# Optimization experiments

Measured on AMD Instinct MI355X. Metric: run time of the kernel, lower is better.

Reference implementation:

```python
import jax, jax.numpy as jnp
import numpy as np

B, N, D = 8, 1024, 1024
H, DH = 16, 64
INNER = H * DH  # == D by construction
MLP = 4096
EPS = 1e-5


def layernorm(x, g, b):
    mu = jnp.mean(x, axis=-1, keepdims=True)
    var = jnp.mean(jnp.square(x - mu), axis=-1, keepdims=True)
    return (x - mu) * jax.lax.rsqrt(var + EPS) * g + b


def setup_inputs() -> dict:
    key = jax.random.key(0)
    ks = jax.random.split(key, 10)
    s = lambda fan_in: 1.0 / np.sqrt(fan_in)
    return {
        "x": jax.random.normal(ks[0], (B, N, D), jnp.float32),
        "ln1_g": jnp.ones((D,), jnp.float32),
        "ln1_b": jnp.zeros((D,), jnp.float32),
        "w_qkv": jax.random.uniform(ks[1], (D, 3 * INNER), jnp.float32, -s(D), s(D)),
        "w_out": jax.random.uniform(ks[2], (INNER, D), jnp.float32, -s(INNER), s(INNER)),
        "b_out": jnp.zeros((D,), jnp.float32),
        "ln2_g": jnp.ones((D,), jnp.float32),
        "ln2_b": jnp.zeros((D,), jnp.float32),
        "w1": jax.random.uniform(ks[3], (D, MLP), jnp.float32, -s(D), s(D)),
        "b1": jnp.zeros((MLP,), jnp.float32),
        "w2": jax.random.uniform(ks[4], (MLP, D), jnp.float32, -s(MLP), s(MLP)),
        "b2": jnp.zeros((D,), jnp.float32),
    }


def reference(x, ln1_g, ln1_b, w_qkv, w_out, b_out, ln2_g, ln2_b, w1, b1, w2, b2):
    scale = DH ** -0.5
    xn = layernorm(x, ln1_g, ln1_b)
    qkv = xn @ w_qkv  # [B, N, 3*INNER]
    embed_dim = xn.shape[-1]
    # faithful to source: slice by embed_dim (== INNER here)
    q, k, v = (qkv[:, :, embed_dim * i: embed_dim * (i + 1)] for i in range(3))
    reshape_heads = lambda t: t.reshape(B, N, H, DH).transpose(0, 2, 1, 3)  # b h n d
    q, k, v = reshape_heads(q), reshape_heads(k), reshape_heads(v)
    scores = jnp.einsum("bhnd,bhmd->bhnm", q, k) * scale
    attn = jax.nn.softmax(scores, axis=-1)
    attn_out = jnp.einsum("bhnm,bhmd->bhnd", attn, v)
    attn_out = attn_out.transpose(0, 2, 1, 3).reshape(B, N, INNER)
    x2 = attn_out @ w_out + b_out  # to_ff projection (project_out=True)
    # feed_forward: LayerNorm -> Linear -> GELU(exact) -> Linear (dropout=0)
    h = layernorm(x2, ln2_g, ln2_b) @ w1 + b1
    h = jax.nn.gelu(h, approximate=False)
    out = h @ w2 + b2
    return out
```

## Files before the change

### kernel.cpp

```cpp
#include <hip/hip_runtime.h>
#include <hip/hip_bf16.h>
#include <math.h>

typedef __bf16 bf16;
typedef __bf16 bf16x8 __attribute__((ext_vector_type(8)));
typedef float f32x4 __attribute__((ext_vector_type(4)));

#define SEQ 1024
#define DMODEL 1024

__device__ __forceinline__ void gld_lds16(const bf16* g, bf16* l) {
    __builtin_amdgcn_global_load_lds(
        (const __attribute__((address_space(1))) unsigned int*)g,
        (__attribute__((address_space(3))) unsigned int*)l, 16, 0, 0);
}

__global__ void transpose_f2b(const float* __restrict__ in, bf16* __restrict__ out,
                              int K, int N) {
    __shared__ float tile[32][33];
    int n0 = blockIdx.x * 32, k0 = blockIdx.y * 32;
    int tx = threadIdx.x, ty = threadIdx.y;
#pragma unroll
    for (int i = 0; i < 4; ++i) {
        int kk = ty + i * 8;
        tile[kk][tx] = in[(size_t)(k0 + kk) * N + n0 + tx];
    }
    __syncthreads();
#pragma unroll
    for (int i = 0; i < 4; ++i) {
        int nn = ty + i * 8;
        out[(size_t)(n0 + nn) * K + k0 + tx] = (bf16)tile[tx][nn];
    }
}

__global__ void ln_f2b(const float* __restrict__ x, const float* __restrict__ g,
                       const float* __restrict__ bta, bf16* __restrict__ y) {
    int row = blockIdx.x, t = threadIdx.x;
    const float* xr = x + (size_t)row * DMODEL;
    float v[4];
#pragma unroll
    for (int i = 0; i < 4; ++i) v[i] = xr[t * 4 + i];
    float s = v[0] + v[1] + v[2] + v[3];
    float s2 = v[0] * v[0] + v[1] * v[1] + v[2] * v[2] + v[3] * v[3];
#pragma unroll
    for (int off = 32; off > 0; off >>= 1) {
        s += __shfl_down(s, off, 64);
        s2 += __shfl_down(s2, off, 64);
    }
    __shared__ float ws1[4], ws2[4];
    __shared__ float mu_s, rstd_s;
    int lane = t & 63, wv = t >> 6;
    if (lane == 0) { ws1[wv] = s; ws2[wv] = s2; }
    __syncthreads();
    if (t == 0) {
        float S1 = ws1[0] + ws1[1] + ws1[2] + ws1[3];
        float S2 = ws2[0] + ws2[1] + ws2[2] + ws2[3];
        float mu = S1 * (1.0f / DMODEL);
        float var = S2 * (1.0f / DMODEL) - mu * mu;
        mu_s = mu;
        rstd_s = rsqrtf(var + 1e-5f);
    }
    __syncthreads();
    float mu = mu_s, rstd = rstd_s;
    bf16* yr = y + (size_t)row * DMODEL;
#pragma unroll
    for (int i = 0; i < 4; ++i) {
        int d = t * 4 + i;
        float o = (v[i] - mu) * rstd * g[d] + bta[d];
        yr[d] = (bf16)o;
    }
}

#define BM 128
#define BN 128
#define BK 32

__global__ __launch_bounds__(256, 2) void gemm_bt(
    const bf16* __restrict__ A, const bf16* __restrict__ Bt,
    const float* __restrict__ bias, void* __restrict__ Cv,
    int M, int N, int K, int mode) {
    __shared__ bf16 sA[BM * BK];
    __shared__ bf16 sB[BN * BK];
    int t = threadIdx.x;
    int lane = t & 63, wave = t >> 6;
    int wr = wave >> 1, wc = wave & 1;
    int m0 = blockIdx.y * BM, n0 = blockIdx.x * BN;
    const bf16* Ap = A + (size_t)m0 * K;
    const bf16* Bp = Bt + (size_t)n0 * K;

    int srow = wave * 16 + (lane >> 2);
    int schunk = lane & 3;
    int gcoff = (schunk ^ (srow & 3)) * 8;
    const bf16* gA0 = Ap + (size_t)srow * K + gcoff;
    const bf16* gA1 = Ap + (size_t)(srow + 64) * K + gcoff;
    const bf16* gB0 = Bp + (size_t)srow * K + gcoff;
    const bf16* gB1 = Bp + (size_t)(srow + 64) * K + gcoff;
    bf16* lA0 = sA + wave * 512;
    bf16* lA1 = sA + 2048 + wave * 512;
    bf16* lB0 = sB + wave * 512;
    bf16* lB1 = sB + 2048 + wave * 512;

    f32x4 acc[4][4];
#pragma unroll
    for (int i = 0; i < 4; ++i)
#pragma unroll
        for (int j = 0; j < 4; ++j) acc[i][j] = (f32x4){0.f, 0.f, 0.f, 0.f};

    int mq = lane & 15, quad = lane >> 4;
    int csw = (quad ^ (mq & 3)) * 8;

    for (int k0 = 0; k0 < K; k0 += BK) {
        __syncthreads();
        gld_lds16(gA0 + k0, lA0);
        gld_lds16(gA1 + k0, lA1);
        gld_lds16(gB0 + k0, lB0);
        gld_lds16(gB1 + k0, lB1);
        __syncthreads();
        bf16x8 af[4], bfr[4];
#pragma unroll
        for (int i = 0; i < 4; ++i)
            af[i] = *(const bf16x8*)&sA[(wr * 64 + i * 16 + mq) * BK + csw];
#pragma unroll
        for (int j = 0; j < 4; ++j)
            bfr[j] = *(const bf16x8*)&sB[(wc * 64 + j * 16 + mq) * BK + csw];
#pragma unroll
        for (int i = 0; i < 4; ++i)
#pragma unroll
            for (int j = 0; j < 4; ++j)
                acc[i][j] = __builtin_amdgcn_mfma_f32_16x16x32_bf16(af[i], bfr[j], acc[i][j], 0, 0, 0);
    }

    int cq = lane & 15, rq = (lane >> 4) * 4;
#pragma unroll
    for (int i = 0; i < 4; ++i) {
        int row = m0 + wr * 64 + i * 16 + rq;
#pragma unroll
        for (int j = 0; j < 4; ++j) {
            int col = n0 + wc * 64 + j * 16 + cq;
            float bv = bias ? bias[col] : 0.0f;
#pragma unroll
            for (int r = 0; r < 4; ++r) {
                float v = acc[i][j][r] + bv;
                if (mode == 1) v = 0.5f * v * (1.0f + erff(v * 0.70710678118654752f));
                size_t idx = (size_t)(row + r) * N + col;
                if (mode == 2) ((float*)Cv)[idx] = v;
                else           ((bf16*)Cv)[idx] = (bf16)v;
            }
        }
    }
}

#define GBAR() do { asm volatile("" ::: "memory"); __builtin_amdgcn_sched_barrier(0); \
    __builtin_amdgcn_s_barrier(); __builtin_amdgcn_sched_barrier(0); asm volatile("" ::: "memory"); } while (0)
#define GWAITV2() do { asm volatile("s_waitcnt vmcnt(2)" ::: "memory"); __builtin_amdgcn_sched_barrier(0); } while (0)
#define GWAITV0() do { asm volatile("s_waitcnt vmcnt(0)" ::: "memory"); __builtin_amdgcn_sched_barrier(0); } while (0)

__global__ __launch_bounds__(512, 2) void gemm256_bt(
    const bf16* __restrict__ A, const bf16* __restrict__ Bt,
    const float* __restrict__ bias, void* __restrict__ Cv,
    int M, int N, int K, int mode) {
    extern __shared__ bf16 smem[];
    int t = threadIdx.x;
    int lane = t & 63, wave = t >> 6;
    int wr = wave >> 2, wc = wave & 3;

    int nbx = gridDim.x;
    int nwg = nbx * (int)gridDim.y;
    int bid = (int)blockIdx.y * nbx + (int)blockIdx.x;
    int qd = nwg >> 3, rm = nwg & 7;
    int xcd = bid & 7, loc = bid >> 3;
    int wg = (xcd < rm ? xcd * (qd + 1) : rm * (qd + 1) + (xcd - rm) * qd) + loc;
    int m0 = (wg / nbx) * 256, n0 = (wg % nbx) * 256;

    const bf16* Ap = A + (size_t)m0 * K;
    const bf16* Bp = Bt + (size_t)n0 * K;

    int sr = lane >> 3;
    int g8 = lane & 7;
    int soff = (g8 ^ (sr & 7)) * 8;
    const bf16* gA = Ap + (size_t)(wave * 8 + sr) * K + soff;
    const bf16* gB = Bp + (size_t)(wave * 8 + sr) * K + soff;

    int mq = lane & 15, quad = lane >> 4;
    int fro = (quad ^ (mq & 7)) * 8;

    f32x4 acc[8][4];
#pragma unroll
    for (int i = 0; i < 8; ++i)
#pragma unroll
        for (int j = 0; j < 4; ++j) acc[i][j] = (f32x4){0.f, 0.f, 0.f, 0.f};

    bf16x8 af[4][2], bq[2][2];
    const bf16 *sA, *sB;
    int nt = K >> 6;

#define SMP(b, ab) (smem + ((size_t)((b) * 2 + (ab))) * 16384)
#define STG(b, cl, tt) do { \
    gld_lds16(gA + (size_t)(cl) * 64 * K + (size_t)(tt) * 64, SMP(b, 0) + ((cl) * 64 + wave * 8) * 64); \
    gld_lds16(gB + (size_t)(cl) * 64 * K + (size_t)(tt) * 64, SMP(b, 1) + ((cl) * 64 + wave * 8) * 64); \
} while (0)
#define LDA(ih) do { _Pragma("unroll") for (int i = 0; i < 4; ++i) { \
    int rw = wr * 128 + (ih) * 64 + i * 16 + mq; \
    af[i][0] = *(const bf16x8*)&sA[rw * 64 + fro]; \
    af[i][1] = *(const bf16x8*)&sA[rw * 64 + (fro ^ 32)]; } } while (0)
#define LDB(jh) do { _Pragma("unroll") for (int j = 0; j < 2; ++j) { \
    int rw = wc * 64 + (jh) * 32 + j * 16 + mq; \
    bq[j][0] = *(const bf16x8*)&sB[rw * 64 + fro]; \
    bq[j][1] = *(const bf16x8*)&sB[rw * 64 + (fro ^ 32)]; } } while (0)
#define MM(ih, jh) do { __builtin_amdgcn_s_setprio(1); \
    _Pragma("unroll") for (int j = 0; j < 2; ++j) \
    _Pragma("unroll") for (int i = 0; i < 4; ++i) { \
        acc[(ih) * 4 + i][(jh) * 2 + j] = __builtin_amdgcn_mfma_f32_16x16x32_bf16( \
            af[i][0], bq[j][0], acc[(ih) * 4 + i][(jh) * 2 + j], 0, 0, 0); \
        acc[(ih) * 4 + i][(jh) * 2 + j] = __builtin_amdgcn_mfma_f32_16x16x32_bf16( \
            af[i][1], bq[j][1], acc[(ih) * 4 + i][(jh) * 2 + j], 0, 0, 0); } \
    __builtin_amdgcn_s_setprio(0); } while (0)

#pragma unroll
    for (int cl = 0; cl < 4; ++cl) STG(0, cl, 0);
    if (nt > 1) { STG(1, 0, 1); GWAITV2(); } else { GWAITV0(); }
    GBAR();

    for (int tt = 0; tt < nt; ++tt) {
        int b = tt & 1;
        sA = SMP(b, 0);
        sB = SMP(b, 1);
        int pf = (tt + 1 < nt);
        LDA(0); LDB(0);
        if (pf) STG(b ^ 1, 1, tt + 1);
        GBAR();
        MM(0, 0);
        GBAR();
        LDB(1);
        if (pf) STG(b ^ 1, 2, tt + 1);
        GBAR();
        MM(0, 1);
        GBAR();
        LDA(1);
        if (pf) STG(b ^ 1, 3, tt + 1);
        GBAR();
        MM(1, 1);
        GBAR();
        LDB(0);
        GBAR();
        MM(1, 0);
        GBAR();
        if (pf) {
            if (tt + 2 < nt) { STG(b, 0, tt + 2); GWAITV2(); }
            else             { GWAITV0(); }
            GBAR();
        }
    }

#undef SMP
#undef STG
#undef LDA
#undef LDB
#undef MM

    int cq = lane & 15, rq = (lane >> 4) * 4;
#pragma unroll
    for (int i = 0; i < 8; ++i) {
        int row = m0 + wr * 128 + i * 16 + rq;
#pragma unroll
        for (int j = 0; j < 4; ++j) {
            int col = n0 + wc * 64 + j * 16 + cq;
            float bv = bias ? bias[col] : 0.0f;
#pragma unroll
            for (int r = 0; r < 4; ++r) {
                float v = acc[i][j][r] + bv;
                if (mode == 1) v = 0.5f * v * (1.0f + erff(v * 0.70710678118654752f));
                size_t idx = (size_t)(row + r) * N + col;
                if (mode == 2) ((float*)Cv)[idx] = v;
                else           ((bf16*)Cv)[idx] = (bf16)v;
            }
        }
    }
}

#define KVB 128
#define LDK2 72
#define LDP 136

__global__ __launch_bounds__(256, 2) void attn_mfma(const bf16* __restrict__ qkv,
                                                    bf16* __restrict__ ao) {
    __shared__ bf16 Klds[KVB][LDK2];
    __shared__ bf16 Vtlds[64][LDP];
    __shared__ bf16 Plds[4][16][LDP];
    int t = threadIdx.x, lane = t & 63, wave = t >> 6;

    int f = (int)blockIdx.y * (int)gridDim.x + (int)blockIdx.x;
    int wg = (f & 7) * 256 + (f >> 3);
    int bh = wg >> 4, bb = bh >> 4, h = bh & 15;
    int q0 = (wg & 15) * 64;

    const bf16* base = qkv + (size_t)bb * SEQ * 3072;
    int m = lane & 15, quad = lane >> 4;
    int kq = quad * 8;

    bf16x8 qf[2];
    {
        int qrow = q0 + wave * 16 + m;
        const bf16* p = base + (size_t)qrow * 3072 + h * 64;
#pragma unroll
        for (int c = 0; c < 2; ++c) {
            bf16x8 tmp = *(const bf16x8*)(p + c * 32 + kq);
#pragma unroll
            for (int j = 0; j < 8; ++j) qf[c][j] = (bf16)((float)tmp[j] * 0.125f);
        }
    }

    float m_run[4], l_run[4];
    f32x4 o_acc[4];
#pragma unroll
    for (int r = 0; r < 4; ++r) { m_run[r] = -3e38f; l_run[r] = 0.f; }
#pragma unroll
    for (int g = 0; g < 4; ++g) o_acc[g] = (f32x4){0.f, 0.f, 0.f, 0.f};

    int skey = t >> 3, sd0 = (t & 7) * 8;
    int rot = t & 7;
    const bf16* pk0 = base + (size_t)skey * 3072 + 1024 + h * 64 + sd0;
    const bf16* pv0 = base + (size_t)skey * 3072 + 2048 + h * 64 + sd0;

    bf16x8 kreg[4], vreg[4];

#define LOADKV(kt2) do { \
    const bf16* pk = pk0 + (size_t)(kt2) * KVB * 3072; \
    const bf16* pv = pv0 + (size_t)(kt2) * KVB * 3072; \
    _Pragma("unroll") for (int c = 0; c < 4; ++c) { \
        kreg[c] = *(const bf16x8*)(pk + (size_t)c * 32 * 3072); \
        vreg[c] = *(const bf16x8*)(pv + (size_t)c * 32 * 3072); } \
} while (0)
#define WRITEKV() do { \
    _Pragma("unroll") for (int c = 0; c < 4; ++c) { \
        *(bf16x8*)&Klds[skey + c * 32][sd0] = kreg[c]; \
        _Pragma("unroll") for (int ii = 0; ii < 8; ++ii) { \
            int j = (ii + rot) & 7; \
            Vtlds[sd0 + j][skey + c * 32] = vreg[c][j]; } } \
} while (0)

    LOADKV(0);
    WRITEKV();
    __syncthreads();

    for (int kt = 0; kt < SEQ / KVB; ++kt) {
        if (kt + 1 < SEQ / KVB) LOADKV(kt + 1);

        f32x4 s[8];
#pragma unroll
        for (int g = 0; g < 8; ++g) {
            bf16x8 b0 = *(const bf16x8*)&Klds[g * 16 + m][kq];
            bf16x8 b1 = *(const bf16x8*)&Klds[g * 16 + m][32 + kq];
            s[g] = (f32x4){0.f, 0.f, 0.f, 0.f};
            s[g] = __builtin_amdgcn_mfma_f32_16x16x32_bf16(qf[0], b0, s[g], 0, 0, 0);
            s[g] = __builtin_amdgcn_mfma_f32_16x16x32_bf16(qf[1], b1, s[g], 0, 0, 0);
        }

#pragma unroll
        for (int r = 0; r < 4; ++r) {
            float mx = s[0][r];
#pragma unroll
            for (int g = 1; g < 8; ++g) mx = fmaxf(mx, s[g][r]);
#pragma unroll
            for (int msk = 1; msk < 16; msk <<= 1) mx = fmaxf(mx, __shfl_xor(mx, msk, 64));
            float m_new = fmaxf(m_run[r], mx);
            float alpha = __expf(m_run[r] - m_new);
            m_run[r] = m_new;
            float rowsum = 0.f;
#pragma unroll
            for (int g = 0; g < 8; ++g) {
                float p = __expf(s[g][r] - m_new);
                s[g][r] = p;
                rowsum += p;
            }
#pragma unroll
            for (int msk = 1; msk < 16; msk <<= 1) rowsum += __shfl_xor(rowsum, msk, 64);
            l_run[r] = l_run[r] * alpha + rowsum;
#pragma unroll
            for (int g = 0; g < 4; ++g) o_acc[g][r] *= alpha;
        }

#pragma unroll
        for (int g = 0; g < 8; ++g)
#pragma unroll
            for (int r = 0; r < 4; ++r)
                Plds[wave][quad * 4 + r][g * 16 + m] = (bf16)s[g][r];

#pragma unroll
        for (int kc = 0; kc < 4; ++kc) {
            bf16x8 pf = *(const bf16x8*)&Plds[wave][m][kc * 32 + kq];
#pragma unroll
            for (int dg = 0; dg < 4; ++dg) {
                bf16x8 vf = *(const bf16x8*)&Vtlds[dg * 16 + m][kc * 32 + kq];
                o_acc[dg] = __builtin_amdgcn_mfma_f32_16x16x32_bf16(pf, vf, o_acc[dg], 0, 0, 0);
            }
        }

        __syncthreads();
        if (kt + 1 < SEQ / KVB) {
            WRITEKV();
        }
        __syncthreads();
    }

#undef LOADKV
#undef WRITEKV

#pragma unroll
    for (int r = 0; r < 4; ++r) {
        int row = q0 + wave * 16 + quad * 4 + r;
        float rl = 1.0f / l_run[r];
        bf16* op = ao + ((size_t)bb * SEQ + row) * DMODEL + h * 64;
#pragma unroll
        for (int g = 0; g < 4; ++g) op[g * 16 + m] = (bf16)(o_acc[g][r] * rl);
    }
}

extern "C" void kernel_launch(void* const* d_in, const int* in_sizes, int n_in,
                              void* d_out, int out_size, void* d_ws, size_t ws_size,
                              hipStream_t stream) {
    const float* x     = (const float*)d_in[0];
    const float* ln1_g = (const float*)d_in[1];
    const float* ln1_b = (const float*)d_in[2];
    const float* w_qkv = (const float*)d_in[3];
    const float* w_out = (const float*)d_in[4];
    const float* b_out = (const float*)d_in[5];
    const float* ln2_g = (const float*)d_in[6];
    const float* ln2_b = (const float*)d_in[7];
    const float* w1    = (const float*)d_in[8];
    const float* b1    = (const float*)d_in[9];
    const float* w2    = (const float*)d_in[10];
    const float* b2    = (const float*)d_in[11];
    float* out = (float*)d_out;
    char* ws = (char*)d_ws;
    char* outc = (char*)d_out;

    static bool lds_init = false;
    if (!lds_init) {
        hipFuncSetAttribute((const void*)gemm256_bt,
                            hipFuncAttributeMaxDynamicSharedMemorySize, 131072);
        lds_init = true;
    }

    bf16* wqkvT = (bf16*)(ws + (0ull << 20));
    bf16* woutT = (bf16*)(ws + (6ull << 20));
    bf16* qkv   = (bf16*)(ws + (8ull << 20));
    bf16* w1T   = (bf16*)(ws + (8ull << 20));
    bf16* w2T   = (bf16*)(ws + (16ull << 20));
    float* x2   = (float*)(ws + (24ull << 20));
    bf16* hbuf  = (bf16*)(ws + (24ull << 20));
    bf16* xn    = (bf16*)(outc + 0);
    bf16* ao    = (bf16*)(outc + 0);
    bf16* x2n   = (bf16*)(outc + (16ull << 20));

    dim3 tb(32, 8);
    transpose_f2b<<<dim3(3072 / 32, 1024 / 32), tb, 0, stream>>>(w_qkv, wqkvT, 1024, 3072);
    transpose_f2b<<<dim3(1024 / 32, 1024 / 32), tb, 0, stream>>>(w_out, woutT, 1024, 1024);

    ln_f2b<<<8192, 256, 0, stream>>>(x, ln1_g, ln1_b, xn);
    gemm256_bt<<<dim3(3072 / 256, 8192 / 256), 512, 131072, stream>>>(xn, wqkvT, nullptr, qkv,
                                                                      8192, 3072, 1024, 0);
    attn_mfma<<<dim3(SEQ / 64, 128), 256, 0, stream>>>(qkv, ao);

    transpose_f2b<<<dim3(4096 / 32, 1024 / 32), tb, 0, stream>>>(w1, w1T, 1024, 4096);
    transpose_f2b<<<dim3(1024 / 32, 4096 / 32), tb, 0, stream>>>(w2, w2T, 4096, 1024);

    gemm_bt<<<dim3(1024 / 128, 8192 / 128), 256, 0, stream>>>(ao, woutT, b_out, x2,
                                                              8192, 1024, 1024, 2);
    ln_f2b<<<8192, 256, 0, stream>>>(x2, ln2_g, ln2_b, x2n);

    for (int c = 0; c < 2; ++c) {
        const bf16* a1 = x2n + (size_t)c * 4096 * 1024;
        float* oc = out + (size_t)c * 4096 * 1024;
        gemm256_bt<<<dim3(4096 / 256, 4096 / 256), 512, 131072, stream>>>(a1, w1T, b1, hbuf,
                                                                          4096, 4096, 1024, 1);
        gemm_bt<<<dim3(1024 / 128, 4096 / 128), 256, 0, stream>>>(hbuf, w2T, b2, oc,
                                                                  4096, 1024, 4096, 2);
    }
}
```

Measured before the change: 697.6 us.

## Transpose attention score MFMA and drop 256-tile GEMM kernel

The attention kernel swaps the MFMA operand order so each lane holds one query row's scores across registers. Row max and sum reductions then need only two cross-quad shuffles instead of four-step butterflies per row, and P is written to LDS as packed 4-element vectors. Separately, the 256x256 pipelined GEMM kernel is removed and the QKV and MLP-up GEMMs revert to the 128-tile gemm_bt kernel. That second change likely gives up the larger tile's data reuse and its load/compute overlap on the two largest GEMMs.

```diff
diff --git a/kernel.cpp b/kernel.cpp
--- a/kernel.cpp
+++ b/kernel.cpp
@@ -3,6 +3,7 @@
 #include <math.h>
 
 typedef __bf16 bf16;
+typedef __bf16 bf16x4 __attribute__((ext_vector_type(4)));
 typedef __bf16 bf16x8 __attribute__((ext_vector_type(8)));
 typedef float f32x4 __attribute__((ext_vector_type(4)));
 
@@ -150,134 +151,6 @@
     }
 }
 
-#define GBAR() do { asm volatile("" ::: "memory"); __builtin_amdgcn_sched_barrier(0); \
-    __builtin_amdgcn_s_barrier(); __builtin_amdgcn_sched_barrier(0); asm volatile("" ::: "memory"); } while (0)
-#define GWAITV2() do { asm volatile("s_waitcnt vmcnt(2)" ::: "memory"); __builtin_amdgcn_sched_barrier(0); } while (0)
-#define GWAITV0() do { asm volatile("s_waitcnt vmcnt(0)" ::: "memory"); __builtin_amdgcn_sched_barrier(0); } while (0)
-
-__global__ __launch_bounds__(512, 2) void gemm256_bt(
-    const bf16* __restrict__ A, const bf16* __restrict__ Bt,
-    const float* __restrict__ bias, void* __restrict__ Cv,
-    int M, int N, int K, int mode) {
-    extern __shared__ bf16 smem[];
-    int t = threadIdx.x;
-    int lane = t & 63, wave = t >> 6;
-    int wr = wave >> 2, wc = wave & 3;
-
-    int nbx = gridDim.x;
-    int nwg = nbx * (int)gridDim.y;
-    int bid = (int)blockIdx.y * nbx + (int)blockIdx.x;
-    int qd = nwg >> 3, rm = nwg & 7;
-    int xcd = bid & 7, loc = bid >> 3;
-    int wg = (xcd < rm ? xcd * (qd + 1) : rm * (qd + 1) + (xcd - rm) * qd) + loc;
-    int m0 = (wg / nbx) * 256, n0 = (wg % nbx) * 256;
-
-    const bf16* Ap = A + (size_t)m0 * K;
-    const bf16* Bp = Bt + (size_t)n0 * K;
-
-    int sr = lane >> 3;
-    int g8 = lane & 7;
-    int soff = (g8 ^ (sr & 7)) * 8;
-    const bf16* gA = Ap + (size_t)(wave * 8 + sr) * K + soff;
-    const bf16* gB = Bp + (size_t)(wave * 8 + sr) * K + soff;
-
-    int mq = lane & 15, quad = lane >> 4;
-    int fro = (quad ^ (mq & 7)) * 8;
-
-    f32x4 acc[8][4];
-#pragma unroll
-    for (int i = 0; i < 8; ++i)
-#pragma unroll
-        for (int j = 0; j < 4; ++j) acc[i][j] = (f32x4){0.f, 0.f, 0.f, 0.f};
-
-    bf16x8 af[4][2], bq[2][2];
-    const bf16 *sA, *sB;
-    int nt = K >> 6;
-
-#define SMP(b, ab) (smem + ((size_t)((b) * 2 + (ab))) * 16384)
-#define STG(b, cl, tt) do { \
-    gld_lds16(gA + (size_t)(cl) * 64 * K + (size_t)(tt) * 64, SMP(b, 0) + ((cl) * 64 + wave * 8) * 64); \
-    gld_lds16(gB + (size_t)(cl) * 64 * K + (size_t)(tt) * 64, SMP(b, 1) + ((cl) * 64 + wave * 8) * 64); \
-} while (0)
-#define LDA(ih) do { _Pragma("unroll") for (int i = 0; i < 4; ++i) { \
-    int rw = wr * 128 + (ih) * 64 + i * 16 + mq; \
-    af[i][0] = *(const bf16x8*)&sA[rw * 64 + fro]; \
-    af[i][1] = *(const bf16x8*)&sA[rw * 64 + (fro ^ 32)]; } } while (0)
-#define LDB(jh) do { _Pragma("unroll") for (int j = 0; j < 2; ++j) { \
-    int rw = wc * 64 + (jh) * 32 + j * 16 + mq; \
-    bq[j][0] = *(const bf16x8*)&sB[rw * 64 + fro]; \
-    bq[j][1] = *(const bf16x8*)&sB[rw * 64 + (fro ^ 32)]; } } while (0)
-#define MM(ih, jh) do { __builtin_amdgcn_s_setprio(1); \
-    _Pragma("unroll") for (int j = 0; j < 2; ++j) \
-    _Pragma("unroll") for (int i = 0; i < 4; ++i) { \
-        acc[(ih) * 4 + i][(jh) * 2 + j] = __builtin_amdgcn_mfma_f32_16x16x32_bf16( \
-            af[i][0], bq[j][0], acc[(ih) * 4 + i][(jh) * 2 + j], 0, 0, 0); \
-        acc[(ih) * 4 + i][(jh) * 2 + j] = __builtin_amdgcn_mfma_f32_16x16x32_bf16( \
-            af[i][1], bq[j][1], acc[(ih) * 4 + i][(jh) * 2 + j], 0, 0, 0); } \
-    __builtin_amdgcn_s_setprio(0); } while (0)
-
-#pragma unroll
-    for (int cl = 0; cl < 4; ++cl) STG(0, cl, 0);
-    if (nt > 1) { STG(1, 0, 1); GWAITV2(); } else { GWAITV0(); }
-    GBAR();
-
-    for (int tt = 0; tt < nt; ++tt) {
-        int b = tt & 1;
-        sA = SMP(b, 0);
-        sB = SMP(b, 1);
-        int pf = (tt + 1 < nt);
-        LDA(0); LDB(0);
-        if (pf) STG(b ^ 1, 1, tt + 1);
-        GBAR();
-        MM(0, 0);
-        GBAR();
-        LDB(1);
-        if (pf) STG(b ^ 1, 2, tt + 1);
-        GBAR();
-        MM(0, 1);
-        GBAR();
-        LDA(1);
-        if (pf) STG(b ^ 1, 3, tt + 1);
-        GBAR();
-        MM(1, 1);
-        GBAR();
-        LDB(0);
-        GBAR();
-        MM(1, 0);
-        GBAR();
-        if (pf) {
-            if (tt + 2 < nt) { STG(b, 0, tt + 2); GWAITV2(); }
-            else             { GWAITV0(); }
-            GBAR();
-        }
-    }
-
-#undef SMP
-#undef STG
-#undef LDA
-#undef LDB
-#undef MM
-
-    int cq = lane & 15, rq = (lane >> 4) * 4;
-#pragma unroll
-    for (int i = 0; i < 8; ++i) {
-        int row = m0 + wr * 128 + i * 16 + rq;
-#pragma unroll
-        for (int j = 0; j < 4; ++j) {
-            int col = n0 + wc * 64 + j * 16 + cq;
-            float bv = bias ? bias[col] : 0.0f;
-#pragma unroll
-            for (int r = 0; r < 4; ++r) {
-                float v = acc[i][j][r] + bv;
-                if (mode == 1) v = 0.5f * v * (1.0f + erff(v * 0.70710678118654752f));
-                size_t idx = (size_t)(row + r) * N + col;
-                if (mode == 2) ((float*)Cv)[idx] = v;
-                else           ((bf16*)Cv)[idx] = (bf16)v;
-            }
-        }
-    }
-}
-
 #define KVB 128
 #define LDK2 72
 #define LDP 136
@@ -310,10 +183,8 @@
         }
     }
 
-    float m_run[4], l_run[4];
+    float m_run = -3e38f, l_run = 0.f;
     f32x4 o_acc[4];
-#pragma unroll
-    for (int r = 0; r < 4; ++r) { m_run[r] = -3e38f; l_run[r] = 0.f; }
 #pragma unroll
     for (int g = 0; g < 4; ++g) o_acc[g] = (f32x4){0.f, 0.f, 0.f, 0.f};
 
@@ -352,39 +223,47 @@
             bf16x8 b0 = *(const bf16x8*)&Klds[g * 16 + m][kq];
             bf16x8 b1 = *(const bf16x8*)&Klds[g * 16 + m][32 + kq];
             s[g] = (f32x4){0.f, 0.f, 0.f, 0.f};
-            s[g] = __builtin_amdgcn_mfma_f32_16x16x32_bf16(qf[0], b0, s[g], 0, 0, 0);
-            s[g] = __builtin_amdgcn_mfma_f32_16x16x32_bf16(qf[1], b1, s[g], 0, 0, 0);
-        }
-
-#pragma unroll
-        for (int r = 0; r < 4; ++r) {
-            float mx = s[0][r];
-#pragma unroll
-            for (int g = 1; g < 8; ++g) mx = fmaxf(mx, s[g][r]);
-#pragma unroll
-            for (int msk = 1; msk < 16; msk <<= 1) mx = fmaxf(mx, __shfl_xor(mx, msk, 64));
-            float m_new = fmaxf(m_run[r], mx);
-            float alpha = __expf(m_run[r] - m_new);
-            m_run[r] = m_new;
-            float rowsum = 0.f;
-#pragma unroll
-            for (int g = 0; g < 8; ++g) {
-                float p = __expf(s[g][r] - m_new);
-                s[g][r] = p;
-                rowsum += p;
-            }
-#pragma unroll
-            for (int msk = 1; msk < 16; msk <<= 1) rowsum += __shfl_xor(rowsum, msk, 64);
-            l_run[r] = l_run[r] * alpha + rowsum;
-#pragma unroll
-            for (int g = 0; g < 4; ++g) o_acc[g][r] *= alpha;
-        }
-
-#pragma unroll
-        for (int g = 0; g < 8; ++g)
-#pragma unroll
-            for (int r = 0; r < 4; ++r)
-                Plds[wave][quad * 4 + r][g * 16 + m] = (bf16)s[g][r];
+            s[g] = __builtin_amdgcn_mfma_f32_16x16x32_bf16(b0, qf[0], s[g], 0, 0, 0);
+            s[g] = __builtin_amdgcn_mfma_f32_16x16x32_bf16(b1, qf[1], s[g], 0, 0, 0);
+        }
+
+        {
+            float mx = s[0][0];
+#pragma unroll
+            for (int g = 0; g < 8; ++g)
+#pragma unroll
+                for (int r = 0; r < 4; ++r) mx = fmaxf(mx, s[g][r]);
+            mx = fmaxf(mx, __shfl_xor(mx, 16, 64));
+            mx = fmaxf(mx, __shfl_xor(mx, 32, 64));
+            float m_new = fmaxf(m_run, mx);
+            float alpha = __expf(m_run - m_new);
+            m_run = m_new;
+            float rs = 0.f;
+#pragma unroll
+            for (int g = 0; g < 8; ++g)
+#pragma unroll
+                for (int r = 0; r < 4; ++r) {
+                    float p = __expf(s[g][r] - m_new);
+                    s[g][r] = p;
+                    rs += p;
+                }
+            rs += __shfl_xor(rs, 16, 64);
+            rs += __shfl_xor(rs, 32, 64);
+            l_run = l_run * alpha + rs;
+            float av[4];
+#pragma unroll
+            for (int r = 0; r < 4; ++r) av[r] = __shfl(alpha, quad * 4 + r, 64);
+#pragma unroll
+            for (int g = 0; g < 4; ++g)
+#pragma unroll
+                for (int r = 0; r < 4; ++r) o_acc[g][r] *= av[r];
+        }
+
+#pragma unroll
+        for (int g = 0; g < 8; ++g) {
+            bf16x4 pw = {(bf16)s[g][0], (bf16)s[g][1], (bf16)s[g][2], (bf16)s[g][3]};
+            *(bf16x4*)&Plds[wave][m][g * 16 + quad * 4] = pw;
+        }
 
 #pragma unroll
         for (int kc = 0; kc < 4; ++kc) {
@@ -409,7 +288,7 @@
 #pragma unroll
     for (int r = 0; r < 4; ++r) {
         int row = q0 + wave * 16 + quad * 4 + r;
-        float rl = 1.0f / l_run[r];
+        float rl = 1.0f / __shfl(l_run, quad * 4 + r, 64);
         bf16* op = ao + ((size_t)bb * SEQ + row) * DMODEL + h * 64;
 #pragma unroll
         for (int g = 0; g < 4; ++g) op[g * 16 + m] = (bf16)(o_acc[g][r] * rl);
@@ -435,13 +314,6 @@
     char* ws = (char*)d_ws;
     char* outc = (char*)d_out;
 
-    static bool lds_init = false;
-    if (!lds_init) {
-        hipFuncSetAttribute((const void*)gemm256_bt,
-                            hipFuncAttributeMaxDynamicSharedMemorySize, 131072);
-        lds_init = true;
-    }
-
     bf16* wqkvT = (bf16*)(ws + (0ull << 20));
     bf16* woutT = (bf16*)(ws + (6ull << 20));
     bf16* qkv   = (bf16*)(ws + (8ull << 20));
@@ -458,8 +330,8 @@
     transpose_f2b<<<dim3(1024 / 32, 1024 / 32), tb, 0, stream>>>(w_out, woutT, 1024, 1024);
 
     ln_f2b<<<8192, 256, 0, stream>>>(x, ln1_g, ln1_b, xn);
-    gemm256_bt<<<dim3(3072 / 256, 8192 / 256), 512, 131072, stream>>>(xn, wqkvT, nullptr, qkv,
-                                                                      8192, 3072, 1024, 0);
+    gemm_bt<<<dim3(3072 / 128, 8192 / 128), 256, 0, stream>>>(xn, wqkvT, nullptr, qkv,
+                                                              8192, 3072, 1024, 0);
     attn_mfma<<<dim3(SEQ / 64, 128), 256, 0, stream>>>(qkv, ao);
 
     transpose_f2b<<<dim3(4096 / 32, 1024 / 32), tb, 0, stream>>>(w1, w1T, 1024, 4096);
@@ -472,8 +344,8 @@
     for (int c = 0; c < 2; ++c) {
         const bf16* a1 = x2n + (size_t)c * 4096 * 1024;
         float* oc = out + (size_t)c * 4096 * 1024;
-        gemm256_bt<<<dim3(4096 / 256, 4096 / 256), 512, 131072, stream>>>(a1, w1T, b1, hbuf,
-                                                                          4096, 4096, 1024, 1);
+        gemm_bt<<<dim3(4096 / 128, 4096 / 128), 256, 0, stream>>>(a1, w1T, b1, hbuf,
+                                                                  4096, 4096, 1024, 1);
         gemm_bt<<<dim3(1024 / 128, 4096 / 128), 256, 0, stream>>>(hbuf, w2T, b2, oc,
                                                                   4096, 1024, 4096, 2);
     }
```

Result: faster. 623.6 us (-10.6%).
